# Kernel tuning notes

Hardware: AMD Instinct MI355X
Metric: run time of the kernel (lower is better)

Reference implementation:

```python
import jax, jax.numpy as jnp
import numpy as np

N_AGENTS = 2
B, C, H, W = 4, 64, 200, 352


def _conv(x, w, b):
    # x: (n, Cin, H, W), w: (Cout, Cin, 3, 3), 'SAME' padding, stride 1
    y = jax.lax.conv_general_dilated(
        x, w, window_strides=(1, 1), padding='SAME',
        dimension_numbers=('NCHW', 'OIHW', 'NCHW'))
    return y + b[None, :, None, None]


def setup_inputs() -> dict:
    key = jax.random.key(0)
    ks = jax.random.split(key, 4)
    s = 0.05  # small init so sigmoid/tanh stay in useful range
    x = jax.random.normal(ks[0], (N_AGENTS, B, C, H, W), dtype=jnp.float32)
    msg_w = jax.random.normal(ks[1], (C, 2 * C, 3, 3), dtype=jnp.float32) * s
    msg_b = jnp.zeros((C,), jnp.float32)
    gates_w = jax.random.normal(ks[2], (2 * C, 3 * C, 3, 3), dtype=jnp.float32) * s
    gates_b = jnp.zeros((2 * C,), jnp.float32)
    can_w = jax.random.normal(ks[3], (C, 3 * C, 3, 3), dtype=jnp.float32) * s
    can_b = jnp.zeros((C,), jnp.float32)
    return {'x': x, 'msg_w': msg_w, 'msg_b': msg_b,
            'gates_w': gates_w, 'gates_b': gates_b,
            'can_w': can_w, 'can_b': can_b}


def reference(x, msg_w, msg_b, gates_w, gates_b, can_w, can_b):
    # num_iteration=1; only new_x[0] (agent 0's updated feature) is returned,
    # so we compute exactly that path.
    x0, x1 = x[0], x[1]                       # each (B, C, H, W)
    neighbor = jnp.concatenate([x0, x1], axis=1)   # (B, 2C, H, W)
    message = _conv(neighbor, msg_w, msg_b)        # (B, C, H, W)
    agg = 0.5 * (x0 + message)                     # 'avg' over stacked pair
    cat_feat = jnp.concatenate([x0, agg], axis=1)  # (B, 2C, H, W)

    # ConvGRU: batch_first input (1, B, 2C, H, W) -> sequence length B, batch 1
    h0 = jnp.zeros((1, C, H, W), cat_feat.dtype)

    def step(h, inp):
        inp = inp[None]                                     # (1, 2C, H, W)
        comb = jnp.concatenate([inp, h], axis=1)            # (1, 3C, H, W)
        gates = jax.nn.sigmoid(_conv(comb, gates_w, gates_b))
        reset, update = jnp.split(gates, 2, axis=1)         # each (1, C, H, W)
        comb2 = jnp.concatenate([inp, reset * h], axis=1)
        cnm = jnp.tanh(_conv(comb2, can_w, can_b))
        h_next = (1.0 - update) * h + update * cnm
        return h_next, h_next[0]

    _, out = jax.lax.scan(step, h0, cat_feat)  # out: (B, C, H, W)
    return out
```

## Files before the change

kernel.cpp:

```cpp
#include <hip/hip_runtime.h>
#include <math.h>
#include <string.h>

#define HH 200
#define WW 352
#define HWSZ (HH*WW)
#define CHW (64L*HWSZ)

enum { EPI_MSG=0, EPI_GATES=1, EPI_CAND=2 };

typedef __attribute__((ext_vector_type(8))) _Float16 f16x8;
typedef __attribute__((ext_vector_type(4))) float f32x4;
typedef __attribute__((ext_vector_type(4))) unsigned int uint4v;
typedef __attribute__((ext_vector_type(4))) unsigned short ushort4v;

__device__ __forceinline__ unsigned short f2h(float f) {
    _Float16 h = (_Float16)f;
    return __builtin_bit_cast(unsigned short, h);
}
__device__ __forceinline__ float h2f(unsigned short u) {
    return (float)__builtin_bit_cast(_Float16, u);
}

__device__ __forceinline__ void load_lds16(const unsigned short* g,
                                           unsigned short* l) {
    __builtin_amdgcn_global_load_lds(
        (const __attribute__((address_space(1))) unsigned int*)g,
        (__attribute__((address_space(3))) unsigned int*)l, 16, 0, 0);
}

__global__ void prepack_k(const float* __restrict__ mw,
                          const float* __restrict__ gw,
                          const float* __restrict__ cw,
                          unsigned short* __restrict__ pw)
{
    const int MSG_I = 4*18432;
    const int GAT_I = 12*18432;
    const int CAN_I = 6*18432;
    int idx = blockIdx.x*256 + threadIdx.x;
    const float* w; int cin, nkb, rel; unsigned short* base;
    if (idx < MSG_I)              { w=mw; cin=128; nkb=4; rel=idx;              base=pw; }
    else if (idx < MSG_I+GAT_I)   { w=gw; cin=192; nkb=6; rel=idx-MSG_I;        base=pw+73728; }
    else if (idx < MSG_I+GAT_I+CAN_I) { w=cw; cin=192; nkb=6; rel=idx-MSG_I-GAT_I; base=pw+294912; }
    else return;
    int chunk = rel / 18432, r = rel - chunk*18432;
    int j = r & 7, lane = (r >> 3) & 63, cfsh = r >> 9;
    int cf = cfsh & 3, sh = cfsh >> 2;
    int q = lane >> 4, n16 = lane & 15;
    int co_l = cf*16 + n16, ch = q*8 + j;
    int cogrp = chunk / nkb, kb = chunk - cogrp*nkb;
    float f = w[(((long)(cogrp*64 + co_l))*cin + kb*32+ch)*9 + sh];
    base[(size_t)chunk*18432 + r] = f2h(f);
}

__global__ void convert_all_k(const float* __restrict__ x,
                              unsigned short* __restrict__ xb0_all,
                              unsigned short* __restrict__ xb1_all)
{
    int idx = blockIdx.x*256 + threadIdx.x;
    int cp   = idx & 15;
    int rest = idx >> 4;
    int px4  = rest % 17600;
    int r2   = rest / 17600;
    int hb = r2 & 1, ag = (r2 >> 1) & 1, t = r2 >> 2;
    const float* src = x + ((size_t)(ag*4 + t))*CHW
                         + (size_t)(hb*32 + 2*cp)*HWSZ + (size_t)px4*4;
    float4 a = *(const float4*)src;
    float4 b = *(const float4*)(src + HWSZ);
    unsigned int* dst = (unsigned int*)((ag ? xb1_all : xb0_all)
                        + (size_t)t*CHW + (size_t)hb*HWSZ*32) + (size_t)px4*64 + cp;
    dst[0]  = (unsigned)f2h(a.x) | ((unsigned)f2h(b.x) << 16);
    dst[16] = (unsigned)f2h(a.y) | ((unsigned)f2h(b.y) << 16);
    dst[32] = (unsigned)f2h(a.z) | ((unsigned)f2h(b.z) << 16);
    dst[48] = (unsigned)f2h(a.w) | ((unsigned)f2h(b.w) << 16);
}

template<int EPI>
__global__ __launch_bounds__(512, 2)
void conv_mfma_k(const unsigned short* __restrict__ seg0b,
                 const unsigned short* __restrict__ seg1b,
                 const unsigned short* __restrict__ seg2b,
                 int nkb, int nkb_stride, int grp_base,
                 const unsigned short* __restrict__ pw,
                 const float* __restrict__ bias,
                 const unsigned short* e_hb,
                 const unsigned short* __restrict__ e_updb,
                 float* out_f,
                 unsigned short* out_b,
                 unsigned short* out_b2)
{
    __shared__ unsigned short s_in0[612*32];
    __shared__ unsigned short s_in1[612*32];
    __shared__ unsigned short s_w0[9*4*64*8];
    __shared__ unsigned short s_w1[9*4*64*8];

    const int tid  = threadIdx.x;
    const int lane = tid & 63;
    const int wv   = tid >> 6;
    const int n16  = lane & 15;
    const int q    = lane >> 4;

    const int z = blockIdx.z;
    int grp, ts = 0;
    if (EPI == EPI_MSG) { ts = z; grp = 0; } else grp = z + grp_base;

    const unsigned short* s0 = seg0b + (EPI==EPI_MSG ? (size_t)ts*CHW : 0);
    const unsigned short* s1 = seg1b + (EPI==EPI_MSG ? (size_t)ts*CHW : 0);
    unsigned short* ob = out_b;
    if (EPI == EPI_MSG) ob = (ts < 3) ? out_b + (size_t)ts*CHW : out_b2;

    const int x0p = blockIdx.x * 32;
    const int y0  = blockIdx.y * 16;

    int hslot = 0, hoff = 0; bool hok = false;
    if (tid < 400) {
        int hp = tid >> 2, gs = tid & 3;
        int row, col;
        if (hp < 34)      { row = 0;  col = hp; }
        else if (hp < 68) { row = 17; col = hp - 34; }
        else { int k = hp - 68; row = 1 + (k >> 1); col = (k & 1) * 33; }
        int pos = row*34 + col;
        int gy = y0 + row - 1, gx = x0p + col - 1;
        hslot = (pos << 5) + (gs << 3);
        int g = (gs ^ pos ^ (pos >> 2)) & 3;
        if ((unsigned)gy < (unsigned)HH && (unsigned)gx < (unsigned)WW) {
            hok = true;
            hoff = ((gy*WW + gx) << 5) + (g << 3);
        }
    }

    auto srcof = [&](int kb) -> const unsigned short* {
        return ((kb < 2) ? s0 : (kb < 4) ? s1 : seg2b) + (size_t)(kb & 1)*HWSZ*32;
    };

    auto stage = [&](int kb, unsigned short* bin, unsigned short* bw, uint4v& hreg) {
        const unsigned short* src = srcof(kb);
#pragma unroll
        for (int j = 0; j < 4; ++j) {
            const int c    = wv + 8*j;
            const int row  = 1 + (c >> 1);
            const int gy   = y0 + row - 1;
            if ((unsigned)gy < (unsigned)HH) {
                const int colh = c & 1;
                const int p0   = row*34 + 1 + colh*16;
                const int pl   = p0 + (lane >> 2);
                const int g    = ((lane & 3) ^ pl ^ (pl >> 2)) & 3;
                const int gx   = x0p + colh*16 + (lane >> 2);
                load_lds16(src + (((size_t)(gy*WW + gx)) << 5) + (g << 3),
                           &bin[(size_t)p0 << 5]);
            }
        }
        {
            const unsigned short* wsrc = pw + (size_t)(grp*nkb_stride + kb)*18432;
#pragma unroll
            for (int i = 0; i < 5; ++i) {
                const int ch = wv + 8*i;
                if (ch < 36)
                    load_lds16(wsrc + ch*512 + (size_t)lane*8, &bw[(size_t)ch*512]);
            }
        }
        hreg = *(const uint4v*)(src + hoff);
    };

    f32x4 acc[4][4];
#pragma unroll
    for (int cf=0; cf<4; ++cf)
#pragma unroll
        for (int p=0; p<4; ++p) acc[cf][p] = (f32x4){0.f,0.f,0.f,0.f};

    auto compute = [&](const unsigned short* sin, const unsigned short* swt) {
#pragma unroll
        for (int ky = 0; ky < 3; ++ky) {
#pragma unroll
            for (int kx = 0; kx < 3; ++kx) {
                const int sh = ky*3 + kx;
                f16x8 aw[4];
#pragma unroll
                for (int cf = 0; cf < 4; ++cf)
                    aw[cf] = *(const f16x8*)&swt[((sh*4 + cf)*64 + lane)*8];
#pragma unroll
                for (int p = 0; p < 4; ++p) {
                    const int rl = 2*wv + (p >> 1) + ky;
                    const int cl = 16*(p & 1) + n16 + kx;
                    const int pos = rl*34 + cl;
                    const int sw = (q ^ pos ^ (pos >> 2)) & 3;
                    f16x8 bfr = *(const f16x8*)&sin[(pos << 5) + (sw << 3)];
#pragma unroll
                    for (int cf = 0; cf < 4; ++cf)
                        acc[cf][p] = __builtin_amdgcn_mfma_f32_16x16x32_f16(
                                         aw[cf], bfr, acc[cf][p], 0, 0, 0);
                }
            }
        }
    };

    {
        const uint4v z4 = (uint4v){0u,0u,0u,0u};
        for (int i = tid; i < 2448; i += 512) {
            *(uint4v*)&s_in0[(size_t)i*8] = z4;
            *(uint4v*)&s_in1[(size_t)i*8] = z4;
        }
    }
    __syncthreads();

    uint4v h0, h1;
    stage(0, s_in0, s_w0, h0);

    for (int kb = 0; kb < nkb; kb += 2) {
        if (hok) *(uint4v*)&s_in0[hslot] = h0;
        __syncthreads();
        stage(kb + 1, s_in1, s_w1, h1);
        __builtin_amdgcn_sched_barrier(0);
        compute(s_in0, s_w0);
        if (hok) *(uint4v*)&s_in1[hslot] = h1;
        __syncthreads();
        if (kb + 2 < nkb) {
            stage(kb + 2, s_in0, s_w0, h0);
            __builtin_amdgcn_sched_barrier(0);
        }
        compute(s_in1, s_w1);
    }

#pragma unroll
    for (int cf = 0; cf < 4; ++cf) {
        const int half   = cf >> 1;
        const int cobase = grp*64 + cf*16 + q*4;
        const int cmod   = (cf & 1)*16 + q*4;
#pragma unroll
        for (int p = 0; p < 4; ++p) {
            const int row = y0 + 2*wv + (p >> 1);
            const int col = x0p + 16*(p & 1) + n16;
            if (row >= HH) continue;
            const long pix = (long)row*WW + col;
            const size_t iidx = (((size_t)half*HWSZ + pix) << 5) + cmod;
            float v[4];
#pragma unroll
            for (int r = 0; r < 4; ++r) v[r] = acc[cf][p][r] + bias[cobase + r];

            if (EPI == EPI_MSG) {
                ushort4v xv = *(const ushort4v*)&s0[iidx];
                ushort4v s;
#pragma unroll
                for (int r = 0; r < 4; ++r)
                    s[r] = f2h(0.5f*(h2f(xv[r]) + v[r]));
                *(ushort4v*)&ob[iidx] = s;
            } else if (EPI == EPI_GATES) {
                if (grp == 0) {
                    ushort4v hv = e_hb ? *(const ushort4v*)&e_hb[iidx]
                                       : (ushort4v){0,0,0,0};
                    ushort4v s;
#pragma unroll
                    for (int r = 0; r < 4; ++r) {
                        float g = 1.f/(1.f + __expf(-v[r]));
                        s[r] = f2h(g * h2f(hv[r]));
                    }
                    *(ushort4v*)&out_b[iidx] = s;
                } else {
                    ushort4v s;
#pragma unroll
                    for (int r = 0; r < 4; ++r)
                        s[r] = f2h(1.f/(1.f + __expf(-v[r])));
                    *(ushort4v*)&out_b2[iidx] = s;
                }
            } else {
                ushort4v uv = *(const ushort4v*)&e_updb[iidx];
                ushort4v hv = e_hb ? *(const ushort4v*)&e_hb[iidx]
                                   : (ushort4v){0,0,0,0};
                ushort4v s;
#pragma unroll
                for (int r = 0; r < 4; ++r) {
                    float cnm = tanhf(v[r]);
                    float u   = h2f(uv[r]);
                    float hn  = (1.f - u)*h2f(hv[r]) + u*cnm;
                    out_f[(long)(cobase+r)*HWSZ + pix] = hn;
                    s[r] = f2h(hn);
                }
                *(ushort4v*)&out_b[iidx] = s;
            }
        }
    }
}

extern "C" void kernel_launch(void* const* d_in, const int* in_sizes, int n_in,
                              void* d_out, int out_size, void* d_ws, size_t ws_size,
                              hipStream_t stream)
{
    const float* x       = (const float*)d_in[0];
    const float* msg_w   = (const float*)d_in[1];
    const float* msg_b   = (const float*)d_in[2];
    const float* gates_w = (const float*)d_in[3];
    const float* gates_b = (const float*)d_in[4];
    const float* can_w   = (const float*)d_in[5];
    const float* can_b   = (const float*)d_in[6];
    float* out = (float*)d_out;

    unsigned short* W       = (unsigned short*)d_ws;
    unsigned short* xb0_all = W;
    unsigned short* aggb3   = W + 4*CHW;
    unsigned short* rhb     = W + 5*CHW;
    unsigned short* updb    = W + 6*CHW;
    unsigned short* hb      = W + 7*CHW;
    unsigned short* pw      = W + 8*CHW;
    unsigned short* pw_msg  = pw;
    unsigned short* pw_gat  = pw + 73728;
    unsigned short* pw_can  = pw + 294912;

    unsigned short* outU16   = (unsigned short*)d_out;
    unsigned short* xb1_all  = outU16;
    unsigned short* aggbase  = outU16 + 4*CHW;

    prepack_k<<<dim3(1584), dim3(256), 0, stream>>>(msg_w, gates_w, can_w, pw);
    convert_all_k<<<dim3(17600), dim3(256), 0, stream>>>(x, xb0_all, xb1_all);

    conv_mfma_k<EPI_MSG><<<dim3(11,13,4), dim3(512), 0, stream>>>(
        xb0_all, xb1_all, nullptr, 4, 4, 0, pw_msg, msg_b,
        nullptr, nullptr, nullptr, aggbase, aggb3);

    for (int t = 0; t < 4; ++t) {
        const unsigned short* xt  = xb0_all + (size_t)t*CHW;
        const unsigned short* agt = (t < 3) ? aggbase + (size_t)t*CHW : aggb3;
        const unsigned short* hprev = t ? hb : nullptr;

        conv_mfma_k<EPI_GATES><<<dim3(11,13, t ? 2 : 1), dim3(512), 0, stream>>>(
            xt, agt, hb, t ? 6 : 4, 6, t ? 0 : 1, pw_gat, gates_b,
            hprev, nullptr, nullptr, rhb, updb);
        conv_mfma_k<EPI_CAND><<<dim3(11,13,1), dim3(512), 0, stream>>>(
            xt, agt, rhb, t ? 6 : 4, 6, 0, pw_can, can_b,
            hprev, updb, out + (size_t)t*CHW, hb, nullptr);
    }
}
```

Baseline: 463.2 us.

## Halve K-chunk to 16 channels with 16x16x16 MFMA to raise occupancy

Splits each 32-channel K block into two 16-channel chunks, halving LDS input and weight buffers. The MFMA changes from 16x16x32 to 16x16x16, and launch bounds go from 2 to 4 blocks per SM. Out-of-range halo rows and pixels now load from a zero page in global memory instead of zero-filling LDS up front. This trades more pipeline iterations and barriers, plus a lower-throughput MFMA, for higher occupancy and less per-block LDS setup.

```diff
diff --git a/kernel.cpp b/kernel.cpp
--- a/kernel.cpp
+++ b/kernel.cpp
@@ -9,7 +9,7 @@
 
 enum { EPI_MSG=0, EPI_GATES=1, EPI_CAND=2 };
 
-typedef __attribute__((ext_vector_type(8))) _Float16 f16x8;
+typedef __attribute__((ext_vector_type(4))) _Float16 f16x4;
 typedef __attribute__((ext_vector_type(4))) float f32x4;
 typedef __attribute__((ext_vector_type(4))) unsigned int uint4v;
 typedef __attribute__((ext_vector_type(4))) unsigned short ushort4v;
@@ -32,25 +32,31 @@
 __global__ void prepack_k(const float* __restrict__ mw,
                           const float* __restrict__ gw,
                           const float* __restrict__ cw,
-                          unsigned short* __restrict__ pw)
+                          unsigned short* __restrict__ pw,
+                          unsigned short* __restrict__ zp)
 {
-    const int MSG_I = 4*18432;
-    const int GAT_I = 12*18432;
-    const int CAN_I = 6*18432;
+    const int MSG_I = 8*9216;
+    const int GAT_I = 24*9216;
+    const int CAN_I = 12*9216;
+    const int TOTAL = MSG_I + GAT_I + CAN_I;
     int idx = blockIdx.x*256 + threadIdx.x;
-    const float* w; int cin, nkb, rel; unsigned short* base;
-    if (idx < MSG_I)              { w=mw; cin=128; nkb=4; rel=idx;              base=pw; }
-    else if (idx < MSG_I+GAT_I)   { w=gw; cin=192; nkb=6; rel=idx-MSG_I;        base=pw+73728; }
-    else if (idx < MSG_I+GAT_I+CAN_I) { w=cw; cin=192; nkb=6; rel=idx-MSG_I-GAT_I; base=pw+294912; }
-    else return;
-    int chunk = rel / 18432, r = rel - chunk*18432;
-    int j = r & 7, lane = (r >> 3) & 63, cfsh = r >> 9;
+    if (idx >= TOTAL) {
+        int r = idx - TOTAL;
+        if (r < 128) zp[r] = 0;
+        return;
+    }
+    const float* w; int cin, nkc, rel; unsigned short* base;
+    if (idx < MSG_I)              { w=mw; cin=128; nkc=8;  rel=idx;              base=pw; }
+    else if (idx < MSG_I+GAT_I)   { w=gw; cin=192; nkc=12; rel=idx-MSG_I;        base=pw+73728; }
+    else                          { w=cw; cin=192; nkc=12; rel=idx-MSG_I-GAT_I;  base=pw+294912; }
+    int chunk = rel / 9216, r = rel - chunk*9216;
+    int j = r & 3, lane = (r >> 2) & 63, cfsh = r >> 8;
     int cf = cfsh & 3, sh = cfsh >> 2;
     int q = lane >> 4, n16 = lane & 15;
-    int co_l = cf*16 + n16, ch = q*8 + j;
-    int cogrp = chunk / nkb, kb = chunk - cogrp*nkb;
-    float f = w[(((long)(cogrp*64 + co_l))*cin + kb*32+ch)*9 + sh];
-    base[(size_t)chunk*18432 + r] = f2h(f);
+    int co_l = cf*16 + n16, ch = q*4 + j;
+    int cogrp = chunk / nkc, kc = chunk - cogrp*nkc;
+    float f = w[(((long)(cogrp*64 + co_l))*cin + kc*16 + ch)*9 + sh];
+    base[(size_t)chunk*9216 + r] = f2h(f);
 }
 
 __global__ void convert_all_k(const float* __restrict__ x,
@@ -76,12 +82,13 @@
 }
 
 template<int EPI>
-__global__ __launch_bounds__(512, 2)
+__global__ __launch_bounds__(512, 4)
 void conv_mfma_k(const unsigned short* __restrict__ seg0b,
                  const unsigned short* __restrict__ seg1b,
                  const unsigned short* __restrict__ seg2b,
-                 int nkb, int nkb_stride, int grp_base,
+                 int nkc, int nkc_stride, int grp_base,
                  const unsigned short* __restrict__ pw,
+                 const unsigned short* __restrict__ zp,
                  const float* __restrict__ bias,
                  const unsigned short* e_hb,
                  const unsigned short* __restrict__ e_updb,
@@ -89,10 +96,10 @@
                  unsigned short* out_b,
                  unsigned short* out_b2)
 {
-    __shared__ unsigned short s_in0[612*32];
-    __shared__ unsigned short s_in1[612*32];
-    __shared__ unsigned short s_w0[9*4*64*8];
-    __shared__ unsigned short s_w1[9*4*64*8];
+    __shared__ unsigned short s_in0[612*16];
+    __shared__ unsigned short s_in1[612*16];
+    __shared__ unsigned short s_w0[9*4*64*4];
+    __shared__ unsigned short s_w1[9*4*64*4];
 
     const int tid  = threadIdx.x;
     const int lane = tid & 63;
@@ -112,54 +119,57 @@
     const int x0p = blockIdx.x * 32;
     const int y0  = blockIdx.y * 16;
 
-    int hslot = 0, hoff = 0; bool hok = false;
-    if (tid < 400) {
-        int hp = tid >> 2, gs = tid & 3;
+    int hdst = 0, hsig = 0; size_t hsrc = 0; bool hval = false;
+    if (tid < 200) {
+        int pp = tid >> 1, hh = tid & 1;
         int row, col;
-        if (hp < 34)      { row = 0;  col = hp; }
-        else if (hp < 68) { row = 17; col = hp - 34; }
-        else { int k = hp - 68; row = 1 + (k >> 1); col = (k & 1) * 33; }
+        if (pp < 34)      { row = 0;  col = pp; }
+        else if (pp < 68) { row = 17; col = pp - 34; }
+        else { int k = pp - 68; row = 1 + (k >> 1); col = (k & 1) * 33; }
         int pos = row*34 + col;
         int gy = y0 + row - 1, gx = x0p + col - 1;
-        hslot = (pos << 5) + (gs << 3);
-        int g = (gs ^ pos ^ (pos >> 2)) & 3;
+        int sg = (pos >> 2) & 1;
+        hsig = sg;
+        hdst = pos*16 + hh*8;
+        int g = hh ^ sg;
         if ((unsigned)gy < (unsigned)HH && (unsigned)gx < (unsigned)WW) {
-            hok = true;
-            hoff = ((gy*WW + gx) << 5) + (g << 3);
-        }
-    }
-
-    auto srcof = [&](int kb) -> const unsigned short* {
-        return ((kb < 2) ? s0 : (kb < 4) ? s1 : seg2b) + (size_t)(kb & 1)*HWSZ*32;
+            hval = true;
+            hsrc = (size_t)(gy*WW + gx)*32 + (size_t)g*8;
+        }
+    }
+    (void)hsig;
+
+    auto srcof = [&](int kc) -> const unsigned short* {
+        const unsigned short* sp = (kc < 4) ? s0 : (kc < 8) ? s1 : seg2b;
+        return sp + (size_t)((kc >> 1) & 1)*HWSZ*32 + (size_t)(kc & 1)*16;
     };
 
-    auto stage = [&](int kb, unsigned short* bin, unsigned short* bw, uint4v& hreg) {
-        const unsigned short* src = srcof(kb);
-#pragma unroll
-        for (int j = 0; j < 4; ++j) {
-            const int c    = wv + 8*j;
-            const int row  = 1 + (c >> 1);
-            const int gy   = y0 + row - 1;
-            if ((unsigned)gy < (unsigned)HH) {
-                const int colh = c & 1;
-                const int p0   = row*34 + 1 + colh*16;
-                const int pl   = p0 + (lane >> 2);
-                const int g    = ((lane & 3) ^ pl ^ (pl >> 2)) & 3;
-                const int gx   = x0p + colh*16 + (lane >> 2);
-                load_lds16(src + (((size_t)(gy*WW + gx)) << 5) + (g << 3),
-                           &bin[(size_t)p0 << 5]);
+    auto stage = [&](int kc, unsigned short* bin, unsigned short* bw, uint4v& hreg) {
+        const unsigned short* src = srcof(kc);
+#pragma unroll
+        for (int i = 0; i < 2; ++i) {
+            const int r  = 1 + wv*2 + i;
+            const int gy = y0 + r - 1;
+            const int pr = lane >> 1;
+            const int pos = r*34 + 1 + pr;
+            const int g = (lane & 1) ^ ((pos >> 2) & 1);
+            const unsigned short* sp = ((unsigned)gy < (unsigned)HH)
+                ? src + ((size_t)(gy*WW + x0p + pr))*32 + (size_t)g*8
+                : zp;
+            load_lds16(sp, &bin[(size_t)(r*34 + 1)*16]);
+        }
+        {
+            const unsigned short* wsrc = pw + (size_t)(grp*nkc_stride + kc)*9216;
+#pragma unroll
+            for (int i = 0; i < 3; ++i) {
+                const int u = wv + 8*i;
+                if (u < 18)
+                    load_lds16(wsrc + (size_t)u*512 + (size_t)lane*8,
+                               &bw[(size_t)u*512]);
             }
         }
-        {
-            const unsigned short* wsrc = pw + (size_t)(grp*nkb_stride + kb)*18432;
-#pragma unroll
-            for (int i = 0; i < 5; ++i) {
-                const int ch = wv + 8*i;
-                if (ch < 36)
-                    load_lds16(wsrc + ch*512 + (size_t)lane*8, &bw[(size_t)ch*512]);
-            }
-        }
-        hreg = *(const uint4v*)(src + hoff);
+        if (tid < 200)
+            hreg = *(const uint4v*)(hval ? src + hsrc : zp);
     };
 
     f32x4 acc[4][4];
@@ -174,48 +184,39 @@
 #pragma unroll
             for (int kx = 0; kx < 3; ++kx) {
                 const int sh = ky*3 + kx;
-                f16x8 aw[4];
+                f16x4 aw[4];
 #pragma unroll
                 for (int cf = 0; cf < 4; ++cf)
-                    aw[cf] = *(const f16x8*)&swt[((sh*4 + cf)*64 + lane)*8];
+                    aw[cf] = *(const f16x4*)&swt[((sh*4 + cf)*64 + lane)*4];
 #pragma unroll
                 for (int p = 0; p < 4; ++p) {
                     const int rl = 2*wv + (p >> 1) + ky;
                     const int cl = 16*(p & 1) + n16 + kx;
                     const int pos = rl*34 + cl;
-                    const int sw = (q ^ pos ^ (pos >> 2)) & 3;
-                    f16x8 bfr = *(const f16x8*)&sin[(pos << 5) + (sw << 3)];
+                    const int h = (q >> 1) ^ ((pos >> 2) & 1);
+                    const f16x4 bfr = *(const f16x4*)&sin[(size_t)pos*16 + h*8 + (q & 1)*4];
 #pragma unroll
                     for (int cf = 0; cf < 4; ++cf)
-                        acc[cf][p] = __builtin_amdgcn_mfma_f32_16x16x32_f16(
+                        acc[cf][p] = __builtin_amdgcn_mfma_f32_16x16x16f16(
                                          aw[cf], bfr, acc[cf][p], 0, 0, 0);
                 }
             }
         }
     };
 
-    {
-        const uint4v z4 = (uint4v){0u,0u,0u,0u};
-        for (int i = tid; i < 2448; i += 512) {
-            *(uint4v*)&s_in0[(size_t)i*8] = z4;
-            *(uint4v*)&s_in1[(size_t)i*8] = z4;
-        }
-    }
-    __syncthreads();
-
     uint4v h0, h1;
     stage(0, s_in0, s_w0, h0);
 
-    for (int kb = 0; kb < nkb; kb += 2) {
-        if (hok) *(uint4v*)&s_in0[hslot] = h0;
+    for (int kc = 0; kc < nkc; kc += 2) {
+        if (tid < 200) *(uint4v*)&s_in0[hdst] = h0;
         __syncthreads();
-        stage(kb + 1, s_in1, s_w1, h1);
+        stage(kc + 1, s_in1, s_w1, h1);
         __builtin_amdgcn_sched_barrier(0);
         compute(s_in0, s_w0);
-        if (hok) *(uint4v*)&s_in1[hslot] = h1;
+        if (tid < 200) *(uint4v*)&s_in1[hdst] = h1;
         __syncthreads();
-        if (kb + 2 < nkb) {
-            stage(kb + 2, s_in0, s_w0, h0);
+        if (kc + 2 < nkc) {
+            stage(kc + 2, s_in0, s_w0, h0);
             __builtin_amdgcn_sched_barrier(0);
         }
         compute(s_in1, s_w1);
@@ -304,16 +305,17 @@
     unsigned short* pw_msg  = pw;
     unsigned short* pw_gat  = pw + 73728;
     unsigned short* pw_can  = pw + 294912;
+    unsigned short* zp      = pw + 405504;
 
     unsigned short* outU16   = (unsigned short*)d_out;
     unsigned short* xb1_all  = outU16;
     unsigned short* aggbase  = outU16 + 4*CHW;
 
-    prepack_k<<<dim3(1584), dim3(256), 0, stream>>>(msg_w, gates_w, can_w, pw);
+    prepack_k<<<dim3(1585), dim3(256), 0, stream>>>(msg_w, gates_w, can_w, pw, zp);
     convert_all_k<<<dim3(17600), dim3(256), 0, stream>>>(x, xb0_all, xb1_all);
 
     conv_mfma_k<EPI_MSG><<<dim3(11,13,4), dim3(512), 0, stream>>>(
-        xb0_all, xb1_all, nullptr, 4, 4, 0, pw_msg, msg_b,
+        xb0_all, xb1_all, nullptr, 8, 8, 0, pw_msg, zp, msg_b,
         nullptr, nullptr, nullptr, aggbase, aggb3);
 
     for (int t = 0; t < 4; ++t) {
@@ -322,10 +324,10 @@
         const unsigned short* hprev = t ? hb : nullptr;
 
         conv_mfma_k<EPI_GATES><<<dim3(11,13, t ? 2 : 1), dim3(512), 0, stream>>>(
-            xt, agt, hb, t ? 6 : 4, 6, t ? 0 : 1, pw_gat, gates_b,
+            xt, agt, hb, t ? 12 : 8, 12, t ? 0 : 1, pw_gat, zp, gates_b,
             hprev, nullptr, nullptr, rhb, updb);
         conv_mfma_k<EPI_CAND><<<dim3(11,13,1), dim3(512), 0, stream>>>(
-            xt, agt, rhb, t ? 6 : 4, 6, 0, pw_can, can_b,
+            xt, agt, rhb, t ? 12 : 8, 12, 0, pw_can, zp, can_b,
             hprev, updb, out + (size_t)t*CHW, hb, nullptr);
     }
 }
```

Result: slower. 916.5 us (+97.9%).

## Halve conv tile height, single-buffer weights, and replace LDS zeroing with zero-page halo

Applied to the files above, without the earlier changes.

The conv block shrinks from 512 threads covering 16 rows to 256 threads covering 8 rows, so there are more blocks (grid y goes from 13 to 25). Weights now sit in one LDS buffer that is reloaded after each compute, behind extra barriers, instead of being double-buffered. Halo loads read from a small zero page in global memory when out of bounds, which removes the LDS clear at kernel start. Together these cut LDS per block to allow more resident blocks and better wave balance across CUs. The cost is more halo overhead per output, since a 10-row tile carries a 2-row halo, plus weight loads that are no longer overlapped with compute.

```diff
diff --git a/kernel.cpp b/kernel.cpp
--- a/kernel.cpp
+++ b/kernel.cpp
@@ -32,24 +32,30 @@
 __global__ void prepack_k(const float* __restrict__ mw,
                           const float* __restrict__ gw,
                           const float* __restrict__ cw,
-                          unsigned short* __restrict__ pw)
+                          unsigned short* __restrict__ pw,
+                          unsigned short* __restrict__ zp)
 {
     const int MSG_I = 4*18432;
     const int GAT_I = 12*18432;
     const int CAN_I = 6*18432;
+    const int TOTAL = MSG_I + GAT_I + CAN_I;
     int idx = blockIdx.x*256 + threadIdx.x;
+    if (idx >= TOTAL) {
+        int r = idx - TOTAL;
+        if (r < 128) zp[r] = 0;
+        return;
+    }
     const float* w; int cin, nkb, rel; unsigned short* base;
     if (idx < MSG_I)              { w=mw; cin=128; nkb=4; rel=idx;              base=pw; }
     else if (idx < MSG_I+GAT_I)   { w=gw; cin=192; nkb=6; rel=idx-MSG_I;        base=pw+73728; }
-    else if (idx < MSG_I+GAT_I+CAN_I) { w=cw; cin=192; nkb=6; rel=idx-MSG_I-GAT_I; base=pw+294912; }
-    else return;
+    else                          { w=cw; cin=192; nkb=6; rel=idx-MSG_I-GAT_I;  base=pw+294912; }
     int chunk = rel / 18432, r = rel - chunk*18432;
     int j = r & 7, lane = (r >> 3) & 63, cfsh = r >> 9;
     int cf = cfsh & 3, sh = cfsh >> 2;
     int q = lane >> 4, n16 = lane & 15;
     int co_l = cf*16 + n16, ch = q*8 + j;
     int cogrp = chunk / nkb, kb = chunk - cogrp*nkb;
-    float f = w[(((long)(cogrp*64 + co_l))*cin + kb*32+ch)*9 + sh];
+    float f = w[(((long)(cogrp*64 + co_l))*cin + kb*32 + ch)*9 + sh];
     base[(size_t)chunk*18432 + r] = f2h(f);
 }
 
@@ -76,12 +82,13 @@
 }
 
 template<int EPI>
-__global__ __launch_bounds__(512, 2)
+__global__ __launch_bounds__(256, 2)
 void conv_mfma_k(const unsigned short* __restrict__ seg0b,
                  const unsigned short* __restrict__ seg1b,
                  const unsigned short* __restrict__ seg2b,
                  int nkb, int nkb_stride, int grp_base,
                  const unsigned short* __restrict__ pw,
+                 const unsigned short* __restrict__ zp,
                  const float* __restrict__ bias,
                  const unsigned short* e_hb,
                  const unsigned short* __restrict__ e_updb,
@@ -89,10 +96,9 @@
                  unsigned short* out_b,
                  unsigned short* out_b2)
 {
-    __shared__ unsigned short s_in0[612*32];
-    __shared__ unsigned short s_in1[612*32];
-    __shared__ unsigned short s_w0[9*4*64*8];
-    __shared__ unsigned short s_w1[9*4*64*8];
+    __shared__ unsigned short s_in0[340*32];
+    __shared__ unsigned short s_in1[340*32];
+    __shared__ unsigned short s_w[9*4*64*8];
 
     const int tid  = threadIdx.x;
     const int lane = tid & 63;
@@ -110,56 +116,68 @@
     if (EPI == EPI_MSG) ob = (ts < 3) ? out_b + (size_t)ts*CHW : out_b2;
 
     const int x0p = blockIdx.x * 32;
-    const int y0  = blockIdx.y * 16;
-
-    int hslot = 0, hoff = 0; bool hok = false;
-    if (tid < 400) {
-        int hp = tid >> 2, gs = tid & 3;
-        int row, col;
-        if (hp < 34)      { row = 0;  col = hp; }
-        else if (hp < 68) { row = 17; col = hp - 34; }
-        else { int k = hp - 68; row = 1 + (k >> 1); col = (k & 1) * 33; }
-        int pos = row*34 + col;
-        int gy = y0 + row - 1, gx = x0p + col - 1;
-        hslot = (pos << 5) + (gs << 3);
-        int g = (gs ^ pos ^ (pos >> 2)) & 3;
-        if ((unsigned)gy < (unsigned)HH && (unsigned)gx < (unsigned)WW) {
-            hok = true;
-            hoff = ((gy*WW + gx) << 5) + (g << 3);
-        }
+    const int y0  = blockIdx.y * 8;
+
+    int hdst0 = 0, hdst1 = 0; size_t hsrc0 = 0, hsrc1 = 0;
+    bool hval0 = false, hval1 = false;
+    {
+        auto hcalc = [&](int s, int& hdst, size_t& hsrc, bool& hval) {
+            int hp = s >> 2, gs = s & 3;
+            int row, col;
+            if (hp < 34)      { row = 0; col = hp; }
+            else if (hp < 68) { row = 9; col = hp - 34; }
+            else { int k = hp - 68; row = 1 + (k >> 1); col = (k & 1) * 33; }
+            int pos = row*34 + col;
+            int gy = y0 + row - 1, gx = x0p + col - 1;
+            hdst = (pos << 5) + (gs << 3);
+            int g = (gs ^ pos ^ (pos >> 2)) & 3;
+            if ((unsigned)gy < (unsigned)HH && (unsigned)gx < (unsigned)WW) {
+                hval = true;
+                hsrc = ((size_t)(gy*WW + gx) << 5) + (size_t)(g << 3);
+            }
+        };
+        if (tid < 336) hcalc(tid, hdst0, hsrc0, hval0);
+        if (tid < 80)  hcalc(tid + 256, hdst1, hsrc1, hval1);
     }
 
     auto srcof = [&](int kb) -> const unsigned short* {
         return ((kb < 2) ? s0 : (kb < 4) ? s1 : seg2b) + (size_t)(kb & 1)*HWSZ*32;
     };
 
-    auto stage = [&](int kb, unsigned short* bin, unsigned short* bw, uint4v& hreg) {
+    struct HV { uint4v a, b; };
+    auto halo_load = [&](int kb, HV& h) {
         const unsigned short* src = srcof(kb);
+        if (tid < 336) h.a = *(const uint4v*)(hval0 ? src + hsrc0 : zp);
+        if (tid < 80)  h.b = *(const uint4v*)(hval1 ? src + hsrc1 : zp);
+    };
+    auto halo_write = [&](unsigned short* bin, const HV& h) {
+        if (tid < 336) *(uint4v*)&bin[hdst0] = h.a;
+        if (tid < 80)  *(uint4v*)&bin[hdst1] = h.b;
+    };
+
+    auto stage_in = [&](int kb, unsigned short* bin) {
+        const unsigned short* src = srcof(kb);
 #pragma unroll
         for (int j = 0; j < 4; ++j) {
-            const int c    = wv + 8*j;
+            const int c    = wv + 4*j;
             const int row  = 1 + (c >> 1);
+            const int colh = c & 1;
             const int gy   = y0 + row - 1;
-            if ((unsigned)gy < (unsigned)HH) {
-                const int colh = c & 1;
-                const int p0   = row*34 + 1 + colh*16;
-                const int pl   = p0 + (lane >> 2);
-                const int g    = ((lane & 3) ^ pl ^ (pl >> 2)) & 3;
-                const int gx   = x0p + colh*16 + (lane >> 2);
-                load_lds16(src + (((size_t)(gy*WW + gx)) << 5) + (g << 3),
-                           &bin[(size_t)p0 << 5]);
-            }
-        }
-        {
-            const unsigned short* wsrc = pw + (size_t)(grp*nkb_stride + kb)*18432;
-#pragma unroll
-            for (int i = 0; i < 5; ++i) {
-                const int ch = wv + 8*i;
-                if (ch < 36)
-                    load_lds16(wsrc + ch*512 + (size_t)lane*8, &bw[(size_t)ch*512]);
-            }
-        }
-        hreg = *(const uint4v*)(src + hoff);
+            const int p0   = row*34 + 1 + colh*16;
+            const int pl   = p0 + (lane >> 2);
+            const int g    = ((lane & 3) ^ pl ^ (pl >> 2)) & 3;
+            const int gx   = x0p + colh*16 + (lane >> 2);
+            load_lds16(src + (((size_t)(gy*WW + gx)) << 5) + (g << 3),
+                       &bin[(size_t)p0 << 5]);
+        }
+    };
+    auto stage_w = [&](int kb) {
+        const unsigned short* wsrc = pw + (size_t)(grp*nkb_stride + kb)*18432;
+#pragma unroll
+        for (int i = 0; i < 9; ++i) {
+            const int u = wv + 4*i;
+            load_lds16(wsrc + (size_t)u*512 + (size_t)lane*8, &s_w[(size_t)u*512]);
+        }
     };
 
     f32x4 acc[4][4];
@@ -168,7 +186,7 @@
 #pragma unroll
         for (int p=0; p<4; ++p) acc[cf][p] = (f32x4){0.f,0.f,0.f,0.f};
 
-    auto compute = [&](const unsigned short* sin, const unsigned short* swt) {
+    auto compute = [&](const unsigned short* sin) {
 #pragma unroll
         for (int ky = 0; ky < 3; ++ky) {
 #pragma unroll
@@ -177,7 +195,7 @@
                 f16x8 aw[4];
 #pragma unroll
                 for (int cf = 0; cf < 4; ++cf)
-                    aw[cf] = *(const f16x8*)&swt[((sh*4 + cf)*64 + lane)*8];
+                    aw[cf] = *(const f16x8*)&s_w[((sh*4 + cf)*64 + lane)*8];
 #pragma unroll
                 for (int p = 0; p < 4; ++p) {
                     const int rl = 2*wv + (p >> 1) + ky;
@@ -194,31 +212,30 @@
         }
     };
 
-    {
-        const uint4v z4 = (uint4v){0u,0u,0u,0u};
-        for (int i = tid; i < 2448; i += 512) {
-            *(uint4v*)&s_in0[(size_t)i*8] = z4;
-            *(uint4v*)&s_in1[(size_t)i*8] = z4;
-        }
-    }
-    __syncthreads();
-
-    uint4v h0, h1;
-    stage(0, s_in0, s_w0, h0);
+    HV h0, h1;
+    stage_in(0, s_in0);
+    stage_w(0);
+    halo_load(0, h0);
 
     for (int kb = 0; kb < nkb; kb += 2) {
-        if (hok) *(uint4v*)&s_in0[hslot] = h0;
+        halo_write(s_in0, h0);
         __syncthreads();
-        stage(kb + 1, s_in1, s_w1, h1);
+        halo_load(kb + 1, h1);
+        stage_in(kb + 1, s_in1);
         __builtin_amdgcn_sched_barrier(0);
-        compute(s_in0, s_w0);
-        if (hok) *(uint4v*)&s_in1[hslot] = h1;
+        compute(s_in0);
+        __syncthreads();
+        stage_w(kb + 1);
+        halo_write(s_in1, h1);
         __syncthreads();
         if (kb + 2 < nkb) {
-            stage(kb + 2, s_in0, s_w0, h0);
+            halo_load(kb + 2, h0);
+            stage_in(kb + 2, s_in0);
             __builtin_amdgcn_sched_barrier(0);
         }
-        compute(s_in1, s_w1);
+        compute(s_in1);
+        __syncthreads();
+        if (kb + 2 < nkb) stage_w(kb + 2);
     }
 
 #pragma unroll
@@ -304,16 +321,17 @@
     unsigned short* pw_msg  = pw;
     unsigned short* pw_gat  = pw + 73728;
     unsigned short* pw_can  = pw + 294912;
+    unsigned short* zp      = pw + 405504;
 
     unsigned short* outU16   = (unsigned short*)d_out;
     unsigned short* xb1_all  = outU16;
     unsigned short* aggbase  = outU16 + 4*CHW;
 
-    prepack_k<<<dim3(1584), dim3(256), 0, stream>>>(msg_w, gates_w, can_w, pw);
+    prepack_k<<<dim3(1585), dim3(256), 0, stream>>>(msg_w, gates_w, can_w, pw, zp);
     convert_all_k<<<dim3(17600), dim3(256), 0, stream>>>(x, xb0_all, xb1_all);
 
-    conv_mfma_k<EPI_MSG><<<dim3(11,13,4), dim3(512), 0, stream>>>(
-        xb0_all, xb1_all, nullptr, 4, 4, 0, pw_msg, msg_b,
+    conv_mfma_k<EPI_MSG><<<dim3(11,25,4), dim3(256), 0, stream>>>(
+        xb0_all, xb1_all, nullptr, 4, 4, 0, pw_msg, zp, msg_b,
         nullptr, nullptr, nullptr, aggbase, aggb3);
 
     for (int t = 0; t < 4; ++t) {
@@ -321,11 +339,11 @@
         const unsigned short* agt = (t < 3) ? aggbase + (size_t)t*CHW : aggb3;
         const unsigned short* hprev = t ? hb : nullptr;
 
-        conv_mfma_k<EPI_GATES><<<dim3(11,13, t ? 2 : 1), dim3(512), 0, stream>>>(
-            xt, agt, hb, t ? 6 : 4, 6, t ? 0 : 1, pw_gat, gates_b,
+        conv_mfma_k<EPI_GATES><<<dim3(11,25, t ? 2 : 1), dim3(256), 0, stream>>>(
+            xt, agt, hb, t ? 6 : 4, 6, t ? 0 : 1, pw_gat, zp, gates_b,
             hprev, nullptr, nullptr, rhb, updb);
-        conv_mfma_k<EPI_CAND><<<dim3(11,13,1), dim3(512), 0, stream>>>(
-            xt, agt, rhb, t ? 6 : 4, 6, 0, pw_can, can_b,
+        conv_mfma_k<EPI_CAND><<<dim3(11,25,1), dim3(256), 0, stream>>>(
+            xt, agt, rhb, t ? 6 : 4, 6, 0, pw_can, zp, can_b,
             hprev, updb, out + (size_t)t*CHW, hb, nullptr);
     }
 }
```

Result: faster. 428.4 us (-7.5%).
